# Optimization experiments

Measured on AMD Instinct MI355X. Metric: run time of the kernel, lower is better.

The kernel has to match this reference:

```python
import jax, jax.numpy as jnp
import numpy as np

NUM_USERS = 1_000_000
NUM_ITEMS = 500_000
NUM_GENRES = 20
NUM_TAGS = 100
EMBEDDING_DIM = 64
HIDDEN_UNITS = [256, 128, 64]
NUM_CLASSES = 5
BATCH = 16384


def setup_inputs() -> dict:
    key = jax.random.key(0)
    ks = jax.random.split(key, 16)
    deep_in = EMBEDDING_DIM * 2 + NUM_GENRES + NUM_TAGS  # 248
    inp = {
        "user": jax.random.randint(ks[0], (BATCH,), 0, NUM_USERS),
        "item": jax.random.randint(ks[1], (BATCH,), 0, NUM_ITEMS),
        "genre": jax.random.uniform(ks[2], (BATCH, NUM_GENRES), dtype=jnp.float32),
        "tag": jax.random.uniform(ks[3], (BATCH, NUM_TAGS), dtype=jnp.float32),
        # wide Linear(num_users+num_items -> HIDDEN_UNITS[-1]); stored transposed
        # as (vocab, out) so the one-hot matmul becomes a row gather.
        "wide_W": jax.random.normal(ks[4], (NUM_USERS + NUM_ITEMS, HIDDEN_UNITS[-1]), dtype=jnp.float32) * 0.01,
        "wide_b": jnp.zeros((HIDDEN_UNITS[-1],), dtype=jnp.float32),
        "user_emb": jax.random.normal(ks[5], (NUM_USERS, EMBEDDING_DIM), dtype=jnp.float32) * 0.01,
        "item_emb": jax.random.normal(ks[6], (NUM_ITEMS, EMBEDDING_DIM), dtype=jnp.float32) * 0.01,
        "W0": jax.random.normal(ks[7], (deep_in, HIDDEN_UNITS[0]), dtype=jnp.float32) * 0.02,
        "b0": jnp.zeros((HIDDEN_UNITS[0],), dtype=jnp.float32),
        "W1": jax.random.normal(ks[8], (HIDDEN_UNITS[0], HIDDEN_UNITS[1]), dtype=jnp.float32) * 0.02,
        "b1": jnp.zeros((HIDDEN_UNITS[1],), dtype=jnp.float32),
        "W2": jax.random.normal(ks[9], (HIDDEN_UNITS[1], HIDDEN_UNITS[2]), dtype=jnp.float32) * 0.02,
        "b2": jnp.zeros((HIDDEN_UNITS[2],), dtype=jnp.float32),
        "final_W": jax.random.normal(ks[10], (HIDDEN_UNITS[-1] * 2, NUM_CLASSES), dtype=jnp.float32) * 0.02,
        "final_b": jnp.zeros((NUM_CLASSES,), dtype=jnp.float32),
    }
    return inp


def reference(user, item, genre, tag, wide_W, wide_b, user_emb, item_emb,
              W0, b0, W1, b1, W2, b2, final_W, final_b):
    # Wide path: one_hot(user)++one_hot(item) @ W + b  ==  gather+sum of rows.
    wide_out = wide_W[user] + wide_W[NUM_USERS + item] + wide_b  # [B, 64]
    # Deep path (dropout is identity in eval mode).
    u = user_emb[user]   # [B, E]
    v = item_emb[item]   # [B, E]
    h = jnp.concatenate([u, v, genre, tag], axis=1)  # [B, 248]
    h = jax.nn.relu(h @ W0 + b0)
    h = jax.nn.relu(h @ W1 + b1)
    h = jax.nn.relu(h @ W2 + b2)  # [B, 64]
    combined = jnp.concatenate([h, wide_out], axis=1)  # [B, 128]
    logits = combined @ final_W + final_b  # [B, NUM_CLASSES]
    return logits
```

## Files before the change

kernel.cpp:

```cpp
#include <hip/hip_runtime.h>

#define BATCH 16384
#define NU 1000000
#define TBR 64
#define MT 512
#define WSOFF0 0
#define WSOFF1 65536
#define WSOFF2 98304
#define WSREQ  212992

typedef __attribute__((ext_vector_type(8))) short short8;
typedef __attribute__((ext_vector_type(4))) float f32x4;

__device__ __forceinline__ unsigned short f32_bf16(float f) {
    unsigned int u = __float_as_uint(f);
    u += 0x7FFF + ((u >> 16) & 1);
    return (unsigned short)(u >> 16);
}

__device__ __forceinline__ int swz(int row, int byteInRow, int rowStrideB) {
    return row * rowStrideB + (byteInRow ^ ((row & 7) << 4));
}

__device__ __forceinline__ short8 cvt8(float4 a, float4 b) {
    short8 s;
    s[0] = (short)f32_bf16(a.x); s[1] = (short)f32_bf16(a.y);
    s[2] = (short)f32_bf16(a.z); s[3] = (short)f32_bf16(a.w);
    s[4] = (short)f32_bf16(b.x); s[5] = (short)f32_bf16(b.y);
    s[6] = (short)f32_bf16(b.z); s[7] = (short)f32_bf16(b.w);
    return s;
}

__global__ void prep_weights(const float* __restrict__ W0, const float* __restrict__ W1,
                             const float* __restrict__ W2, unsigned short* __restrict__ ws)
{
    __shared__ float t[64 * 65];
    int b = blockIdx.x;
    const float* src; unsigned short* dst; int K, N, K2, k0, n0;
    if (b < 16)      { src = W0; dst = ws + WSOFF0; K = 248; N = 256; K2 = 256; k0 = (b >> 2) * 64; n0 = (b & 3) * 64; }
    else if (b < 24) { int i = b - 16; src = W1; dst = ws + WSOFF1; K = 256; N = 128; K2 = 256; k0 = (i >> 1) * 64; n0 = (i & 1) * 64; }
    else             { int i = b - 24; src = W2; dst = ws + WSOFF2; K = 128; N = 64;  K2 = 128; k0 = i * 64; n0 = 0; }

    int tid = threadIdx.x;
    for (int q = tid; q < 64 * 16; q += 256) {
        int k = q >> 4, nq = q & 15;
        float4 v = make_float4(0.f, 0.f, 0.f, 0.f);
        if (k0 + k < K) v = *(const float4*)(src + (size_t)(k0 + k) * N + n0 + nq * 4);
        t[k * 65 + nq * 4 + 0] = v.x;
        t[k * 65 + nq * 4 + 1] = v.y;
        t[k * 65 + nq * 4 + 2] = v.z;
        t[k * 65 + nq * 4 + 3] = v.w;
    }
    __syncthreads();
    for (int q = tid; q < 64 * 8; q += 256) {
        int n = q >> 3, kg = q & 7;
        short8 o;
        #pragma unroll
        for (int i = 0; i < 8; ++i) o[i] = (short)f32_bf16(t[(kg * 8 + i) * 65 + n]);
        *(short8*)(dst + (size_t)(n0 + n) * K2 + k0 + kg * 8) = o;
    }
}

__global__ __launch_bounds__(MT) void wd_mfma(
        const int* __restrict__ user, const int* __restrict__ item,
        const float* __restrict__ genre, const float* __restrict__ tag,
        const float* __restrict__ wide_W, const float* __restrict__ wide_b,
        const float* __restrict__ user_emb, const float* __restrict__ item_emb,
        const float* __restrict__ b0, const float* __restrict__ b1,
        const float* __restrict__ b2,
        const float* __restrict__ fW, const float* __restrict__ fb,
        const unsigned short* __restrict__ ws, float* __restrict__ out)
{
    __shared__ unsigned short sX[TBR * 256];
    __shared__ unsigned short sH1[TBR * 128];
    __shared__ float sH2[TBR * 68];
    __shared__ float sWide[TBR * 68];

    const int tid = threadIdx.x;
    const int row0 = blockIdx.x * TBR;
    const unsigned short* w0t = ws + WSOFF0;
    const unsigned short* w1t = ws + WSOFF1;
    const unsigned short* w2t = ws + WSOFF2;

    for (int q = tid; q < TBR * 32; q += MT) {
        int r = q >> 5, j = q & 31;
        int grow = row0 + r;
        float4 va = make_float4(0.f, 0.f, 0.f, 0.f);
        float4 vb = va;
        if (j < 8) {
            const float4* p = (const float4*)(user_emb + (size_t)user[grow] * 64);
            va = p[j * 2]; vb = p[j * 2 + 1];
        } else if (j < 16) {
            const float4* p = (const float4*)(item_emb + (size_t)item[grow] * 64);
            va = p[(j - 8) * 2]; vb = p[(j - 8) * 2 + 1];
        } else if (j == 16) {
            const float4* p = (const float4*)(genre + (size_t)grow * 20);
            va = p[0]; vb = p[1];
        } else if (j == 17) {
            const float4* p = (const float4*)(genre + (size_t)grow * 20);
            va = p[2]; vb = p[3];
        } else if (j == 18) {
            va = *(const float4*)(genre + (size_t)grow * 20 + 16);
            vb = *(const float4*)(tag + (size_t)grow * 100);
        } else if (j < 31) {
            const float4* p = (const float4*)(tag + (size_t)grow * 100 + 4);
            int jj = j - 19;
            va = p[jj * 2]; vb = p[jj * 2 + 1];
        }
        *(short8*)((char*)sX + swz(r, j * 16, 512)) = cvt8(va, vb);
    }

    for (int q = tid; q < TBR * 16; q += MT) {
        int r = q >> 4, j = q & 15;
        int grow = row0 + r;
        float4 a = ((const float4*)(wide_W + (size_t)user[grow] * 64))[j];
        float4 b = ((const float4*)(wide_W + (size_t)(NU + item[grow]) * 64))[j];
        float4 c = ((const float4*)wide_b)[j];
        float4 v = make_float4(a.x + b.x + c.x, a.y + b.y + c.y,
                               a.z + b.z + c.z, a.w + b.w + c.w);
        *(float4*)(sWide + r * 68 + j * 4) = v;
    }
    __syncthreads();

    const int wid = tid >> 6;
    const int lane = tid & 63;
    const int lr = lane & 15;
    const int lh = lane >> 4;

    {
        const int cbase = wid * 32;
        f32x4 acc[4][2];
        #pragma unroll
        for (int rt = 0; rt < 4; ++rt)
            #pragma unroll
            for (int t = 0; t < 2; ++t) acc[rt][t] = (f32x4)(0.f);

        for (int kc = 0; kc < 8; ++kc) {
            const int kb = kc * 32 + lh * 8;
            short8 a[4];
            #pragma unroll
            for (int rt = 0; rt < 4; ++rt)
                a[rt] = *(const short8*)((const char*)sX + swz(rt * 16 + lr, kb * 2, 512));
            #pragma unroll
            for (int t = 0; t < 2; ++t) {
                short8 bf = *(const short8*)(w0t + (size_t)(cbase + t * 16 + lr) * 256 + kb);
                #pragma unroll
                for (int rt = 0; rt < 4; ++rt)
                    acc[rt][t] = __builtin_amdgcn_mfma_f32_16x16x32_bf16(a[rt], bf, acc[rt][t], 0, 0, 0);
            }
        }
        __syncthreads();
        #pragma unroll
        for (int t = 0; t < 2; ++t) {
            float bias = b0[cbase + t * 16 + lr];
            #pragma unroll
            for (int rt = 0; rt < 4; ++rt)
                #pragma unroll
                for (int jj = 0; jj < 4; ++jj) {
                    int row = rt * 16 + lh * 4 + jj;
                    float v = fmaxf(acc[rt][t][jj] + bias, 0.f);
                    *(unsigned short*)((char*)sX + swz(row, (cbase + t * 16 + lr) * 2, 512)) = f32_bf16(v);
                }
        }
        __syncthreads();
    }

    {
        const int cbase = wid * 16;
        f32x4 acc[4];
        #pragma unroll
        for (int rt = 0; rt < 4; ++rt) acc[rt] = (f32x4)(0.f);

        for (int kc = 0; kc < 8; ++kc) {
            const int kb = kc * 32 + lh * 8;
            short8 a[4];
            #pragma unroll
            for (int rt = 0; rt < 4; ++rt)
                a[rt] = *(const short8*)((const char*)sX + swz(rt * 16 + lr, kb * 2, 512));
            short8 bf = *(const short8*)(w1t + (size_t)(cbase + lr) * 256 + kb);
            #pragma unroll
            for (int rt = 0; rt < 4; ++rt)
                acc[rt] = __builtin_amdgcn_mfma_f32_16x16x32_bf16(a[rt], bf, acc[rt], 0, 0, 0);
        }
        float bias = b1[cbase + lr];
        #pragma unroll
        for (int rt = 0; rt < 4; ++rt)
            #pragma unroll
            for (int jj = 0; jj < 4; ++jj) {
                int row = rt * 16 + lh * 4 + jj;
                float v = fmaxf(acc[rt][jj] + bias, 0.f);
                *(unsigned short*)((char*)sH1 + swz(row, (cbase + lr) * 2, 256)) = f32_bf16(v);
            }
        __syncthreads();
    }

    {
        const int t = wid & 3;
        const int rtb = (wid >> 2) * 2;
        const int cbase = t * 16;
        f32x4 acc[2];
        acc[0] = (f32x4)(0.f); acc[1] = (f32x4)(0.f);

        for (int kc = 0; kc < 4; ++kc) {
            const int kb = kc * 32 + lh * 8;
            short8 a[2];
            #pragma unroll
            for (int rr = 0; rr < 2; ++rr)
                a[rr] = *(const short8*)((const char*)sH1 + swz((rtb + rr) * 16 + lr, kb * 2, 256));
            short8 bf = *(const short8*)(w2t + (size_t)(cbase + lr) * 128 + kb);
            #pragma unroll
            for (int rr = 0; rr < 2; ++rr)
                acc[rr] = __builtin_amdgcn_mfma_f32_16x16x32_bf16(a[rr], bf, acc[rr], 0, 0, 0);
        }
        float bias = b2[cbase + lr];
        #pragma unroll
        for (int rr = 0; rr < 2; ++rr)
            #pragma unroll
            for (int jj = 0; jj < 4; ++jj) {
                int row = (rtb + rr) * 16 + lh * 4 + jj;
                sH2[row * 68 + cbase + lr] = fmaxf(acc[rr][jj] + bias, 0.f);
            }
        __syncthreads();
    }

    if (tid < TBR * 5) {
        int r = tid / 5, c = tid - r * 5;
        float acc = fb[c];
        #pragma unroll 4
        for (int k = 0; k < 64; ++k) acc = fmaf(sH2[r * 68 + k], fW[k * 5 + c], acc);
        #pragma unroll 4
        for (int k = 0; k < 64; ++k) acc = fmaf(sWide[r * 68 + k], fW[(64 + k) * 5 + c], acc);
        out[(size_t)(row0 + r) * 5 + c] = acc;
    }
}

#define NTHR 256
#define TB 32

__device__ __forceinline__ void fma4(float4& a, float s, const float4& w) {
    a.x = fmaf(s, w.x, a.x); a.y = fmaf(s, w.y, a.y);
    a.z = fmaf(s, w.z, a.z); a.w = fmaf(s, w.w, a.w);
}
__device__ __forceinline__ float4 add4(const float4& a, const float4& b) {
    return make_float4(a.x + b.x, a.y + b.y, a.z + b.z, a.w + b.w);
}
__device__ __forceinline__ float4 relu4(const float4& a) {
    return make_float4(fmaxf(a.x, 0.f), fmaxf(a.y, 0.f), fmaxf(a.z, 0.f), fmaxf(a.w, 0.f));
}

__global__ void wd_fused(const int* __restrict__ user, const int* __restrict__ item,
                         const float* __restrict__ genre, const float* __restrict__ tag,
                         const float* __restrict__ wide_W, const float* __restrict__ wide_b,
                         const float* __restrict__ user_emb, const float* __restrict__ item_emb,
                         const float* __restrict__ W0, const float* __restrict__ b0,
                         const float* __restrict__ W1, const float* __restrict__ b1,
                         const float* __restrict__ W2, const float* __restrict__ b2,
                         const float* __restrict__ fW, const float* __restrict__ fb,
                         float* __restrict__ out)
{
    __shared__ float sA[TB * 248];
    __shared__ float sB[TB * 256];
    __shared__ float sC[TB * 64];

    const int tid = threadIdx.x;
    const int row0 = blockIdx.x * TB;

    for (int q = tid; q < TB * 62; q += NTHR) {
        int r = q / 62, j = q - r * 62, grow = row0 + r;
        float4 v;
        if (j < 16) v = reinterpret_cast<const float4*>(user_emb + (size_t)user[grow] * 64)[j];
        else if (j < 32) v = reinterpret_cast<const float4*>(item_emb + (size_t)item[grow] * 64)[j - 16];
        else if (j < 37) v = reinterpret_cast<const float4*>(genre + (size_t)grow * 20)[j - 32];
        else v = reinterpret_cast<const float4*>(tag + (size_t)grow * 100)[j - 37];
        *reinterpret_cast<float4*>(sA + r * 248 + j * 4) = v;
    }
    for (int q = tid; q < TB * 16; q += NTHR) {
        int r = q >> 4, j = q & 15, grow = row0 + r;
        float4 a = reinterpret_cast<const float4*>(wide_W + (size_t)user[grow] * 64)[j];
        float4 b = reinterpret_cast<const float4*>(wide_W + (size_t)(NU + item[grow]) * 64)[j];
        float4 c = reinterpret_cast<const float4*>(wide_b)[j];
        *reinterpret_cast<float4*>(sC + r * 64 + j * 4) =
            make_float4(a.x + b.x + c.x, a.y + b.y + c.y, a.z + b.z + c.z, a.w + b.w + c.w);
    }
    __syncthreads();
    {
        const int cg = tid & 63, r0 = (tid >> 6) * 8;
        float4 acc[8];
        #pragma unroll
        for (int r = 0; r < 8; ++r) acc[r] = make_float4(0.f, 0.f, 0.f, 0.f);
        for (int k = 0; k < 248; k += 4) {
            const float4* wp = reinterpret_cast<const float4*>(W0 + (size_t)k * 256) + cg;
            float4 w0 = wp[0], w1 = wp[64], w2 = wp[128], w3 = wp[192];
            #pragma unroll
            for (int r = 0; r < 8; ++r) {
                float4 xv = *reinterpret_cast<const float4*>(sA + (r0 + r) * 248 + k);
                fma4(acc[r], xv.x, w0); fma4(acc[r], xv.y, w1);
                fma4(acc[r], xv.z, w2); fma4(acc[r], xv.w, w3);
            }
        }
        float4 bb = reinterpret_cast<const float4*>(b0)[cg];
        #pragma unroll
        for (int r = 0; r < 8; ++r)
            *reinterpret_cast<float4*>(sB + (r0 + r) * 256 + cg * 4) = relu4(add4(acc[r], bb));
    }
    __syncthreads();
    {
        const int cg = tid & 31, r0 = (tid >> 5) * 4;
        float4 acc[4];
        #pragma unroll
        for (int r = 0; r < 4; ++r) acc[r] = make_float4(0.f, 0.f, 0.f, 0.f);
        for (int k = 0; k < 256; k += 4) {
            const float4* wp = reinterpret_cast<const float4*>(W1 + (size_t)k * 128) + cg;
            float4 w0 = wp[0], w1 = wp[32], w2 = wp[64], w3 = wp[96];
            #pragma unroll
            for (int r = 0; r < 4; ++r) {
                float4 xv = *reinterpret_cast<const float4*>(sB + (r0 + r) * 256 + k);
                fma4(acc[r], xv.x, w0); fma4(acc[r], xv.y, w1);
                fma4(acc[r], xv.z, w2); fma4(acc[r], xv.w, w3);
            }
        }
        float4 bb = reinterpret_cast<const float4*>(b1)[cg];
        #pragma unroll
        for (int r = 0; r < 4; ++r)
            *reinterpret_cast<float4*>(sA + (r0 + r) * 128 + cg * 4) = relu4(add4(acc[r], bb));
    }
    __syncthreads();
    {
        const int cg = tid & 15, r0 = (tid >> 4) * 2;
        float4 acc[2];
        acc[0] = make_float4(0.f, 0.f, 0.f, 0.f); acc[1] = acc[0];
        for (int k = 0; k < 128; k += 4) {
            const float4* wp = reinterpret_cast<const float4*>(W2 + (size_t)k * 64) + cg;
            float4 w0 = wp[0], w1 = wp[16], w2 = wp[32], w3 = wp[48];
            #pragma unroll
            for (int r = 0; r < 2; ++r) {
                float4 xv = *reinterpret_cast<const float4*>(sA + (r0 + r) * 128 + k);
                fma4(acc[r], xv.x, w0); fma4(acc[r], xv.y, w1);
                fma4(acc[r], xv.z, w2); fma4(acc[r], xv.w, w3);
            }
        }
        float4 bb = reinterpret_cast<const float4*>(b2)[cg];
        #pragma unroll
        for (int r = 0; r < 2; ++r)
            *reinterpret_cast<float4*>(sB + (r0 + r) * 64 + cg * 4) = relu4(add4(acc[r], bb));
    }
    __syncthreads();
    if (tid < TB * 5) {
        int r = tid / 5, c = tid - r * 5;
        float acc = fb[c];
        for (int k = 0; k < 64; ++k) acc = fmaf(sB[r * 64 + k], fW[k * 5 + c], acc);
        for (int k = 0; k < 64; ++k) acc = fmaf(sC[r * 64 + k], fW[(64 + k) * 5 + c], acc);
        out[(size_t)(row0 + r) * 5 + c] = acc;
    }
}

extern "C" void kernel_launch(void* const* d_in, const int* in_sizes, int n_in,
                              void* d_out, int out_size, void* d_ws, size_t ws_size,
                              hipStream_t stream) {
    const int* user = (const int*)d_in[0];
    const int* item = (const int*)d_in[1];
    const float* genre = (const float*)d_in[2];
    const float* tag = (const float*)d_in[3];
    const float* wide_W = (const float*)d_in[4];
    const float* wide_b = (const float*)d_in[5];
    const float* user_emb = (const float*)d_in[6];
    const float* item_emb = (const float*)d_in[7];
    const float* W0 = (const float*)d_in[8];
    const float* b0 = (const float*)d_in[9];
    const float* W1 = (const float*)d_in[10];
    const float* b1 = (const float*)d_in[11];
    const float* W2 = (const float*)d_in[12];
    const float* b2 = (const float*)d_in[13];
    const float* fW = (const float*)d_in[14];
    const float* fb = (const float*)d_in[15];
    float* out = (float*)d_out;

    if (ws_size >= (size_t)WSREQ) {
        hipLaunchKernelGGL(prep_weights, dim3(26), dim3(256), 0, stream,
                           W0, W1, W2, (unsigned short*)d_ws);
        hipLaunchKernelGGL(wd_mfma, dim3(BATCH / TBR), dim3(MT), 0, stream,
                           user, item, genre, tag, wide_W, wide_b, user_emb, item_emb,
                           b0, b1, b2, fW, fb, (const unsigned short*)d_ws, out);
    } else {
        hipLaunchKernelGGL(wd_fused, dim3(BATCH / TB), dim3(NTHR), 0, stream,
                           user, item, genre, tag, wide_W, wide_b, user_emb, item_emb,
                           W0, b0, W1, b1, W2, b2, fW, fb, out);
    }
}
```

Measured before the change: 32.60 us.

## Halve block row tile, add separate H0 buffer, store H2/wide in bf16 LDS

Cuts rows per block from 64 to 32, doubling the grid to 512 blocks, and gives layer 0 its own LDS output buffer so the sync between its MMA loop and epilogue can go. The H2 and wide activations are now kept in shared memory as bf16 and read eight at a time in the final layer, and the MFMA k-loops are fully unrolled. The aim is more blocks across CUs and less LDS and register pressure per block. The cost is that each block still streams the full weight set for half as many rows, and the wide path loses precision by passing through bf16.

```diff
diff --git a/kernel.cpp b/kernel.cpp
--- a/kernel.cpp
+++ b/kernel.cpp
@@ -2,7 +2,7 @@
 
 #define BATCH 16384
 #define NU 1000000
-#define TBR 64
+#define TBR 32
 #define MT 512
 #define WSOFF0 0
 #define WSOFF1 65536
@@ -10,12 +10,16 @@
 #define WSREQ  212992
 
 typedef __attribute__((ext_vector_type(8))) short short8;
+typedef __attribute__((ext_vector_type(4))) short short4v;
 typedef __attribute__((ext_vector_type(4))) float f32x4;
 
 __device__ __forceinline__ unsigned short f32_bf16(float f) {
     unsigned int u = __float_as_uint(f);
     u += 0x7FFF + ((u >> 16) & 1);
     return (unsigned short)(u >> 16);
+}
+__device__ __forceinline__ float bf16_f32(unsigned short h) {
+    return __uint_as_float(((unsigned int)h) << 16);
 }
 
 __device__ __forceinline__ int swz(int row, int byteInRow, int rowStrideB) {
@@ -72,9 +76,10 @@
         const unsigned short* __restrict__ ws, float* __restrict__ out)
 {
     __shared__ unsigned short sX[TBR * 256];
+    __shared__ unsigned short sH0[TBR * 256];
     __shared__ unsigned short sH1[TBR * 128];
-    __shared__ float sH2[TBR * 68];
-    __shared__ float sWide[TBR * 68];
+    __shared__ unsigned short sH2[TBR * 72];
+    __shared__ unsigned short sWide[TBR * 72];
 
     const int tid = threadIdx.x;
     const int row0 = blockIdx.x * TBR;
@@ -116,9 +121,12 @@
         float4 a = ((const float4*)(wide_W + (size_t)user[grow] * 64))[j];
         float4 b = ((const float4*)(wide_W + (size_t)(NU + item[grow]) * 64))[j];
         float4 c = ((const float4*)wide_b)[j];
-        float4 v = make_float4(a.x + b.x + c.x, a.y + b.y + c.y,
-                               a.z + b.z + c.z, a.w + b.w + c.w);
-        *(float4*)(sWide + r * 68 + j * 4) = v;
+        short4v o;
+        o[0] = (short)f32_bf16(a.x + b.x + c.x);
+        o[1] = (short)f32_bf16(a.y + b.y + c.y);
+        o[2] = (short)f32_bf16(a.z + b.z + c.z);
+        o[3] = (short)f32_bf16(a.w + b.w + c.w);
+        *(short4v*)(sWide + r * 72 + j * 4) = o;
     }
     __syncthreads();
 
@@ -129,37 +137,37 @@
 
     {
         const int cbase = wid * 32;
-        f32x4 acc[4][2];
-        #pragma unroll
-        for (int rt = 0; rt < 4; ++rt)
+        f32x4 acc[2][2];
+        #pragma unroll
+        for (int rt = 0; rt < 2; ++rt)
             #pragma unroll
             for (int t = 0; t < 2; ++t) acc[rt][t] = (f32x4)(0.f);
 
+        #pragma unroll
         for (int kc = 0; kc < 8; ++kc) {
             const int kb = kc * 32 + lh * 8;
-            short8 a[4];
-            #pragma unroll
-            for (int rt = 0; rt < 4; ++rt)
+            short8 a[2];
+            #pragma unroll
+            for (int rt = 0; rt < 2; ++rt)
                 a[rt] = *(const short8*)((const char*)sX + swz(rt * 16 + lr, kb * 2, 512));
             #pragma unroll
             for (int t = 0; t < 2; ++t) {
                 short8 bf = *(const short8*)(w0t + (size_t)(cbase + t * 16 + lr) * 256 + kb);
                 #pragma unroll
-                for (int rt = 0; rt < 4; ++rt)
+                for (int rt = 0; rt < 2; ++rt)
                     acc[rt][t] = __builtin_amdgcn_mfma_f32_16x16x32_bf16(a[rt], bf, acc[rt][t], 0, 0, 0);
             }
         }
-        __syncthreads();
         #pragma unroll
         for (int t = 0; t < 2; ++t) {
             float bias = b0[cbase + t * 16 + lr];
             #pragma unroll
-            for (int rt = 0; rt < 4; ++rt)
+            for (int rt = 0; rt < 2; ++rt)
                 #pragma unroll
                 for (int jj = 0; jj < 4; ++jj) {
                     int row = rt * 16 + lh * 4 + jj;
                     float v = fmaxf(acc[rt][t][jj] + bias, 0.f);
-                    *(unsigned short*)((char*)sX + swz(row, (cbase + t * 16 + lr) * 2, 512)) = f32_bf16(v);
+                    *(unsigned short*)((char*)sH0 + swz(row, (cbase + t * 16 + lr) * 2, 512)) = f32_bf16(v);
                 }
         }
         __syncthreads();
@@ -167,24 +175,24 @@
 
     {
         const int cbase = wid * 16;
-        f32x4 acc[4];
-        #pragma unroll
-        for (int rt = 0; rt < 4; ++rt) acc[rt] = (f32x4)(0.f);
-
+        f32x4 acc[2];
+        acc[0] = (f32x4)(0.f); acc[1] = (f32x4)(0.f);
+
+        #pragma unroll
         for (int kc = 0; kc < 8; ++kc) {
             const int kb = kc * 32 + lh * 8;
-            short8 a[4];
-            #pragma unroll
-            for (int rt = 0; rt < 4; ++rt)
-                a[rt] = *(const short8*)((const char*)sX + swz(rt * 16 + lr, kb * 2, 512));
+            short8 a[2];
+            #pragma unroll
+            for (int rt = 0; rt < 2; ++rt)
+                a[rt] = *(const short8*)((const char*)sH0 + swz(rt * 16 + lr, kb * 2, 512));
             short8 bf = *(const short8*)(w1t + (size_t)(cbase + lr) * 256 + kb);
             #pragma unroll
-            for (int rt = 0; rt < 4; ++rt)
+            for (int rt = 0; rt < 2; ++rt)
                 acc[rt] = __builtin_amdgcn_mfma_f32_16x16x32_bf16(a[rt], bf, acc[rt], 0, 0, 0);
         }
         float bias = b1[cbase + lr];
         #pragma unroll
-        for (int rt = 0; rt < 4; ++rt)
+        for (int rt = 0; rt < 2; ++rt)
             #pragma unroll
             for (int jj = 0; jj < 4; ++jj) {
                 int row = rt * 16 + lh * 4 + jj;
@@ -196,40 +204,43 @@
 
     {
         const int t = wid & 3;
-        const int rtb = (wid >> 2) * 2;
+        const int rtb = wid >> 2;
         const int cbase = t * 16;
-        f32x4 acc[2];
-        acc[0] = (f32x4)(0.f); acc[1] = (f32x4)(0.f);
-
+        f32x4 acc = (f32x4)(0.f);
+
+        #pragma unroll
         for (int kc = 0; kc < 4; ++kc) {
             const int kb = kc * 32 + lh * 8;
-            short8 a[2];
-            #pragma unroll
-            for (int rr = 0; rr < 2; ++rr)
-                a[rr] = *(const short8*)((const char*)sH1 + swz((rtb + rr) * 16 + lr, kb * 2, 256));
+            short8 a = *(const short8*)((const char*)sH1 + swz(rtb * 16 + lr, kb * 2, 256));
             short8 bf = *(const short8*)(w2t + (size_t)(cbase + lr) * 128 + kb);
-            #pragma unroll
-            for (int rr = 0; rr < 2; ++rr)
-                acc[rr] = __builtin_amdgcn_mfma_f32_16x16x32_bf16(a[rr], bf, acc[rr], 0, 0, 0);
+            acc = __builtin_amdgcn_mfma_f32_16x16x32_bf16(a, bf, acc, 0, 0, 0);
         }
         float bias = b2[cbase + lr];
         #pragma unroll
-        for (int rr = 0; rr < 2; ++rr)
-            #pragma unroll
-            for (int jj = 0; jj < 4; ++jj) {
-                int row = (rtb + rr) * 16 + lh * 4 + jj;
-                sH2[row * 68 + cbase + lr] = fmaxf(acc[rr][jj] + bias, 0.f);
-            }
+        for (int jj = 0; jj < 4; ++jj) {
+            int row = rtb * 16 + lh * 4 + jj;
+            sH2[row * 72 + cbase + lr] = f32_bf16(fmaxf(acc[jj] + bias, 0.f));
+        }
         __syncthreads();
     }
 
     if (tid < TBR * 5) {
         int r = tid / 5, c = tid - r * 5;
         float acc = fb[c];
-        #pragma unroll 4
-        for (int k = 0; k < 64; ++k) acc = fmaf(sH2[r * 68 + k], fW[k * 5 + c], acc);
-        #pragma unroll 4
-        for (int k = 0; k < 64; ++k) acc = fmaf(sWide[r * 68 + k], fW[(64 + k) * 5 + c], acc);
+        #pragma unroll
+        for (int kq = 0; kq < 8; ++kq) {
+            short8 h = *(const short8*)(sH2 + r * 72 + kq * 8);
+            #pragma unroll
+            for (int i = 0; i < 8; ++i)
+                acc = fmaf(bf16_f32((unsigned short)h[i]), fW[(kq * 8 + i) * 5 + c], acc);
+        }
+        #pragma unroll
+        for (int kq = 0; kq < 8; ++kq) {
+            short8 h = *(const short8*)(sWide + r * 72 + kq * 8);
+            #pragma unroll
+            for (int i = 0; i < 8; ++i)
+                acc = fmaf(bf16_f32((unsigned short)h[i]), fW[(64 + kq * 8 + i) * 5 + c], acc);
+        }
         out[(size_t)(row0 + r) * 5 + c] = acc;
     }
 }
```

Result: slower. 34.36 us (+5.4%).
